# Optimization experiments

Hardware: AMD Instinct MI355X
Metric: run time of the kernel (lower is better)

The kernel has to match this reference:

```python
import jax, jax.numpy as jnp
import numpy as np

D = 256

def setup_inputs() -> dict:
    key = jax.random.key(0)
    ks = jax.random.split(key, 7)
    B, N = 4, 4096
    s = 1.0 / np.sqrt(D)
    return {
        "x": jax.random.normal(ks[0], (B, D, N), dtype=jnp.float32),
        "Wq": jax.random.normal(ks[1], (D, D), dtype=jnp.float32) * s,
        "bq": jax.random.normal(ks[2], (D,), dtype=jnp.float32) * s,
        "Wk": jax.random.normal(ks[3], (D, D), dtype=jnp.float32) * s,
        "bk": jax.random.normal(ks[4], (D,), dtype=jnp.float32) * s,
        "Wv": jax.random.normal(ks[5], (D, D), dtype=jnp.float32) * s,
        "bv": jax.random.normal(ks[6], (D,), dtype=jnp.float32) * s,
    }


def reference(x, Wq, bq, Wk, bk, Wv, bv):
    # x: (B, D, N) -> xt: (B, N, D)
    xt = jnp.swapaxes(x, 1, 2)
    q = xt @ Wq + bq  # (B, N, D)
    k = xt @ Wk + bk
    v = xt @ Wv + bv
    # full N x N attention, NO 1/sqrt(d) scaling (matches original)
    attn = jnp.einsum("bnd,bmd->bnm", q, k)
    attn = jax.nn.softmax(attn, axis=-1)
    out = jnp.einsum("bnm,bmd->bnd", attn, v)  # (B, N, D)
    return jnp.swapaxes(out, 1, 2)  # (B, D, N)
```

## Files before the change

kernel.cpp:

```cpp
#include <hip/hip_runtime.h>
#include <math.h>

#define Dd 256
#define Nn 4096
#define Bb 4
#define BQ 128
#define BK 128
#define SPLIT 2

typedef _Float16 f16;
typedef _Float16 half8 __attribute__((ext_vector_type(8)));
typedef _Float16 half4 __attribute__((ext_vector_type(4)));
typedef float f32x4 __attribute__((ext_vector_type(4)));

#define LOG2E 1.4426950408889634f

template <int CTRL>
__device__ __forceinline__ float dppf(float x) {
    int r = __builtin_amdgcn_update_dpp(0, __builtin_bit_cast(int, x),
                                        CTRL, 0xF, 0xF, false);
    return __builtin_bit_cast(float, r);
}
__device__ __forceinline__ float red16_max(float x) {
    x = fmaxf(x, dppf<0x128>(x));
    x = fmaxf(x, dppf<0x124>(x));
    x = fmaxf(x, dppf<0x122>(x));
    x = fmaxf(x, dppf<0x121>(x));
    return x;
}
__device__ __forceinline__ float red16_sum(float x) {
    x += dppf<0x128>(x); x += dppf<0x124>(x);
    x += dppf<0x122>(x); x += dppf<0x121>(x);
    return x;
}

__global__ __launch_bounds__(256) void wtrans(
    const float* __restrict__ Wq, const float* __restrict__ Wk,
    const float* __restrict__ Wv, f16* __restrict__ Wt)
{
    __shared__ float ld[64][65];
    const int which = blockIdx.y;
    const float* W = which == 0 ? Wq : (which == 1 ? Wk : Wv);
    const int tr = (blockIdx.x >> 2) * 64;
    const int tc = (blockIdx.x & 3) * 64;
    const int t = threadIdx.x;
    #pragma unroll
    for (int i = 0; i < 16; ++i) {
        int u = t + i * 256, r = u >> 6, c = u & 63;
        ld[r][c] = W[(size_t)(tr + r) * Dd + tc + c];
    }
    __syncthreads();
    f16* Wo = Wt + (size_t)which * Dd * Dd;
    #pragma unroll
    for (int i = 0; i < 16; ++i) {
        int u = t + i * 256, cp = u >> 6, rp = u & 63;
        Wo[(size_t)(tc + cp) * Dd + tr + rp] = (f16)ld[rp][cp];
    }
}

__global__ __launch_bounds__(512, 1) void qkv_fused(
    const float* __restrict__ x, const f16* __restrict__ Wt,
    const float* __restrict__ bq, const float* __restrict__ bk,
    const float* __restrict__ bv,
    f16* __restrict__ Qh, f16* __restrict__ Kh, f16* __restrict__ Vth)
{
    __shared__ __align__(16) f16 Ws[256][264];
    __shared__ float bs3[3][256];
    f16 (*xT)[264] = (f16 (*)[264])&Ws[0][0];

    const int t = threadIdx.x;
    const int wave = t >> 6, lane = t & 63, quad = lane >> 4, l15 = lane & 15;
    const int g = wave & 3;
    const int h = wave >> 2;
    const int n0 = blockIdx.x * 64;
    const int b = blockIdx.y;

    if (t < 256) { bs3[0][t] = bq[t]; bs3[1][t] = bk[t]; bs3[2][t] = bv[t]; }

    const float* xb = x + (size_t)b * Dd * Nn;
    #pragma unroll
    for (int i = 0; i < 8; ++i) {
        int u = t + i * 512, d = u >> 4, nq = (u & 15) * 4;
        float4 v4 = *(const float4*)&xb[(size_t)d * Nn + n0 + nq];
        xT[nq + 0][d] = (f16)v4.x; xT[nq + 1][d] = (f16)v4.y;
        xT[nq + 2][d] = (f16)v4.z; xT[nq + 3][d] = (f16)v4.w;
    }
    __syncthreads();

    half8 a[8];
    #pragma unroll
    for (int c = 0; c < 8; ++c)
        a[c] = *(const half8*)&xT[16 * g + l15][c * 32 + quad * 8];

    const int nrow = n0 + 16 * g + quad * 4;

    for (int which = 0; which < 3; ++which) {
        __syncthreads();

        const f16* Wb = Wt + (size_t)which * Dd * Dd;
        #pragma unroll
        for (int i = 0; i < 16; ++i) {
            int u = t + i * 512;
            int r = u >> 5, c = u & 31;
            *(half8*)&Ws[r][c * 8] = *(const half8*)(Wb + (size_t)r * Dd + c * 8);
        }
        __syncthreads();

        f32x4 acc[8];
        #pragma unroll
        for (int dt = 0; dt < 8; ++dt) acc[dt] = (f32x4){0.f, 0.f, 0.f, 0.f};
        #pragma unroll
        for (int c = 0; c < 8; ++c) {
            #pragma unroll
            for (int dt = 0; dt < 8; ++dt) {
                half8 bfr = *(const half8*)&Ws[h * 128 + dt * 16 + l15][c * 32 + quad * 8];
                acc[dt] = __builtin_amdgcn_mfma_f32_16x16x32_f16(a[c], bfr, acc[dt], 0, 0, 0);
            }
        }

        if (which < 2) {
            f16* O = (which == 0 ? Qh : Kh) + ((size_t)b * Nn + nrow) * Dd;
            #pragma unroll
            for (int dt = 0; dt < 8; ++dt) {
                int col = h * 128 + dt * 16 + l15;
                float bvv = bs3[which][col];
                #pragma unroll
                for (int r = 0; r < 4; ++r)
                    O[(size_t)r * Dd + col] = (f16)(acc[dt][r] + bvv);
            }
        } else {
            f16* O = Vth + (size_t)b * Dd * Nn;
            #pragma unroll
            for (int dt = 0; dt < 8; ++dt) {
                int col = h * 128 + dt * 16 + l15;
                float bvv = bs3[2][col];
                half4 o;
                #pragma unroll
                for (int r = 0; r < 4; ++r) o[r] = (f16)(acc[dt][r] + bvv);
                *(half4*)&O[(size_t)col * Nn + nrow] = o;
            }
        }
    }
}

__global__ __launch_bounds__(512, 2) void attn_mfma(
    const f16* __restrict__ Qh, const f16* __restrict__ Kh,
    const f16* __restrict__ Vth, f16* __restrict__ Opart,
    float* __restrict__ mpart, float* __restrict__ lpart)
{
    __shared__ f16 Ks[BK][264];
    __shared__ f16 Ps[8][16][136];
    __shared__ float alpha_s[8][16];
    __shared__ float l_sh[8][16];

    const int t    = threadIdx.x;
    const int wave = t >> 6, lane = t & 63;
    const int quad = lane >> 4, l15 = lane & 15;
    const int b    = blockIdx.y;
    const int s    = blockIdx.z;
    const int q0   = blockIdx.x * BQ;
    const int qw   = q0 + wave * 16;
    const int kv0  = s * (Nn / SPLIT);

    half8 qf[8];
    const f16* Qrow = Qh + ((size_t)b * Nn + qw + l15) * Dd + quad * 8;
    #pragma unroll
    for (int c = 0; c < 8; ++c) {
        qf[c] = *(const half8*)(Qrow + c * 32);
        qf[c] = qf[c] * (f16)LOG2E;
    }

    f32x4 acc[16];
    #pragma unroll
    for (int n = 0; n < 16; ++n) acc[n] = (f32x4){0.f, 0.f, 0.f, 0.f};
    f32x4 m4 = {-1e30f, -1e30f, -1e30f, -1e30f};
    f32x4 l4 = {0.f, 0.f, 0.f, 0.f};

    const f16* Kb   = Kh + (size_t)b * Nn * Dd;
    const f16* Vrow = Vth + (size_t)b * Dd * Nn
                    + (size_t)(wave * 32 + l15) * Nn + quad * 8;

    for (int k0 = kv0; k0 < kv0 + Nn / SPLIT; k0 += BK) {
        half8 vbf[2][4];
        #pragma unroll
        for (int dt = 0; dt < 2; ++dt) {
            #pragma unroll
            for (int cbb = 0; cbb < 4; ++cbb)
                vbf[dt][cbb] = *(const half8*)(Vrow + (size_t)dt * 16 * Nn + k0 + cbb * 32);
        }

        __syncthreads();

        #pragma unroll
        for (int i = 0; i < 8; ++i) {
            int u = t + i * 512;
            int r = u >> 5, c = u & 31;
            *(half8*)&Ks[r][c * 8] =
                *(const half8*)(Kb + (size_t)(k0 + r) * Dd + c * 8);
        }
        __syncthreads();

        f32x4 S[8];
        #pragma unroll
        for (int cb = 0; cb < 8; ++cb) S[cb] = (f32x4){0.f, 0.f, 0.f, 0.f};
        #pragma unroll
        for (int c = 0; c < 8; ++c) {
            #pragma unroll
            for (int cb = 0; cb < 8; ++cb) {
                half8 kb = *(const half8*)&Ks[cb * 16 + l15][c * 32 + quad * 8];
                S[cb] = __builtin_amdgcn_mfma_f32_16x16x32_f16(qf[c], kb, S[cb], 0, 0, 0);
            }
        }

        f32x4 tmax = S[0];
        #pragma unroll
        for (int cb = 1; cb < 8; ++cb) {
            tmax.x = fmaxf(tmax.x, S[cb].x); tmax.y = fmaxf(tmax.y, S[cb].y);
            tmax.z = fmaxf(tmax.z, S[cb].z); tmax.w = fmaxf(tmax.w, S[cb].w);
        }
        tmax.x = red16_max(tmax.x); tmax.y = red16_max(tmax.y);
        tmax.z = red16_max(tmax.z); tmax.w = red16_max(tmax.w);
        f32x4 newm;
        newm.x = fmaxf(m4.x, tmax.x); newm.y = fmaxf(m4.y, tmax.y);
        newm.z = fmaxf(m4.z, tmax.z); newm.w = fmaxf(m4.w, tmax.w);
        f32x4 al;
        al.x = __builtin_amdgcn_exp2f(m4.x - newm.x);
        al.y = __builtin_amdgcn_exp2f(m4.y - newm.y);
        al.z = __builtin_amdgcn_exp2f(m4.z - newm.z);
        al.w = __builtin_amdgcn_exp2f(m4.w - newm.w);
        f32x4 P[8];
        #pragma unroll
        for (int cb = 0; cb < 8; ++cb) {
            P[cb].x = __builtin_amdgcn_exp2f(S[cb].x - newm.x);
            P[cb].y = __builtin_amdgcn_exp2f(S[cb].y - newm.y);
            P[cb].z = __builtin_amdgcn_exp2f(S[cb].z - newm.z);
            P[cb].w = __builtin_amdgcn_exp2f(S[cb].w - newm.w);
        }
        f32x4 rsum = P[0];
        #pragma unroll
        for (int cb = 1; cb < 8; ++cb) rsum += P[cb];
        rsum.x = red16_sum(rsum.x); rsum.y = red16_sum(rsum.y);
        rsum.z = red16_sum(rsum.z); rsum.w = red16_sum(rsum.w);
        l4 = l4 * al + rsum;
        m4 = newm;

        const int pr = quad * 4;
        #pragma unroll
        for (int cb = 0; cb < 8; ++cb) {
            Ps[wave][pr + 0][cb * 16 + l15] = (f16)P[cb].x;
            Ps[wave][pr + 1][cb * 16 + l15] = (f16)P[cb].y;
            Ps[wave][pr + 2][cb * 16 + l15] = (f16)P[cb].z;
            Ps[wave][pr + 3][cb * 16 + l15] = (f16)P[cb].w;
        }
        if (l15 == 0) {
            float4 a4 = {al.x, al.y, al.z, al.w};
            *(float4*)&alpha_s[wave][pr] = a4;
        }
        __syncthreads();

        float4 alq[8];
        int need = 0;
        #pragma unroll
        for (int qb = 0; qb < 8; ++qb) {
            alq[qb] = *(const float4*)&alpha_s[qb][pr];
            need |= (alq[qb].x != 1.f) | (alq[qb].y != 1.f) |
                    (alq[qb].z != 1.f) | (alq[qb].w != 1.f);
        }
        if (__any(need)) {
            #pragma unroll
            for (int qb = 0; qb < 8; ++qb) {
                f32x4 a = {alq[qb].x, alq[qb].y, alq[qb].z, alq[qb].w};
                acc[qb * 2 + 0] *= a;
                acc[qb * 2 + 1] *= a;
            }
        }

        #pragma unroll
        for (int qb = 0; qb < 8; ++qb) {
            #pragma unroll
            for (int cbb = 0; cbb < 4; ++cbb) {
                half8 ap = *(const half8*)&Ps[qb][l15][cbb * 32 + quad * 8];
                acc[qb * 2 + 0] = __builtin_amdgcn_mfma_f32_16x16x32_f16(
                    ap, vbf[0][cbb], acc[qb * 2 + 0], 0, 0, 0);
                acc[qb * 2 + 1] = __builtin_amdgcn_mfma_f32_16x16x32_f16(
                    ap, vbf[1][cbb], acc[qb * 2 + 1], 0, 0, 0);
            }
        }
    }

    __syncthreads();
    if (l15 == 0) {
        const int pr = quad * 4;
        float4 lv = {l4.x, l4.y, l4.z, l4.w};
        *(float4*)&l_sh[wave][pr] = lv;
        float mv[4] = {m4.x, m4.y, m4.z, m4.w};
        float lvv[4] = {l4.x, l4.y, l4.z, l4.w};
        #pragma unroll
        for (int r = 0; r < 4; ++r) {
            int n = qw + pr + r;
            mpart[(size_t)(s * Bb + b) * Nn + n] = mv[r];
            lpart[(size_t)(s * Bb + b) * Nn + n] = lvv[r];
        }
    }
    __syncthreads();

    f16* Ob = Opart + (size_t)(s * Bb + b) * Dd * Nn;
    #pragma unroll
    for (int qb = 0; qb < 8; ++qb) {
        float4 lq = *(const float4*)&l_sh[qb][quad * 4];
        f32x4 inv = {1.f / lq.x, 1.f / lq.y, 1.f / lq.z, 1.f / lq.w};
        #pragma unroll
        for (int dt = 0; dt < 2; ++dt) {
            int d = wave * 32 + dt * 16 + l15;
            f32x4 o = acc[qb * 2 + dt] * inv;
            half4 oh;
            oh[0] = (f16)o.x; oh[1] = (f16)o.y; oh[2] = (f16)o.z; oh[3] = (f16)o.w;
            *(half4*)&Ob[(size_t)d * Nn + q0 + qb * 16 + quad * 4] = oh;
        }
    }
}

__global__ __launch_bounds__(256) void combine(
    const f16* __restrict__ Opart, const float* __restrict__ mpart,
    const float* __restrict__ lpart, float* __restrict__ out)
{
    const int t = threadIdx.x;
    const int n0 = (blockIdx.x * 256 + t) * 8;
    const int d = blockIdx.y, b = blockIdx.z;

    float m[SPLIT][8], l[SPLIT][8];
    #pragma unroll
    for (int s = 0; s < SPLIT; ++s) {
        size_t base = (size_t)(s * Bb + b) * Nn + n0;
        float4 a0 = *(const float4*)&mpart[base];
        float4 a1 = *(const float4*)&mpart[base + 4];
        float4 c0 = *(const float4*)&lpart[base];
        float4 c1 = *(const float4*)&lpart[base + 4];
        m[s][0]=a0.x; m[s][1]=a0.y; m[s][2]=a0.z; m[s][3]=a0.w;
        m[s][4]=a1.x; m[s][5]=a1.y; m[s][6]=a1.z; m[s][7]=a1.w;
        l[s][0]=c0.x; l[s][1]=c0.y; l[s][2]=c0.z; l[s][3]=c0.w;
        l[s][4]=c1.x; l[s][5]=c1.y; l[s][6]=c1.z; l[s][7]=c1.w;
    }
    float w[SPLIT][8];
    #pragma unroll
    for (int jx = 0; jx < 8; ++jx) {
        float M = m[0][jx];
        #pragma unroll
        for (int s = 1; s < SPLIT; ++s) M = fmaxf(M, m[s][jx]);
        float L = 0.f;
        #pragma unroll
        for (int s = 0; s < SPLIT; ++s) {
            float ws = l[s][jx] * __builtin_amdgcn_exp2f(m[s][jx] - M);
            w[s][jx] = ws; L += ws;
        }
        float invL = 1.f / L;
        #pragma unroll
        for (int s = 0; s < SPLIT; ++s) w[s][jx] *= invL;
    }

    float o[8];
    #pragma unroll
    for (int jx = 0; jx < 8; ++jx) o[jx] = 0.f;
    #pragma unroll
    for (int s = 0; s < SPLIT; ++s) {
        half8 h = *(const half8*)&Opart[((size_t)(s * Bb + b) * Dd + d) * Nn + n0];
        #pragma unroll
        for (int jx = 0; jx < 8; ++jx) o[jx] += w[s][jx] * (float)h[jx];
    }
    float* op = out + ((size_t)b * Dd + d) * Nn + n0;
    f32x4 o0 = {o[0], o[1], o[2], o[3]};
    f32x4 o1 = {o[4], o[5], o[6], o[7]};
    *(f32x4*)op = o0;
    *(f32x4*)(op + 4) = o1;
}

extern "C" void kernel_launch(void* const* d_in, const int* in_sizes, int n_in,
                              void* d_out, int out_size, void* d_ws, size_t ws_size,
                              hipStream_t stream) {
    const float* x  = (const float*)d_in[0];
    const float* Wq = (const float*)d_in[1];
    const float* bq = (const float*)d_in[2];
    const float* Wk = (const float*)d_in[3];
    const float* bk = (const float*)d_in[4];
    const float* Wv = (const float*)d_in[5];
    const float* bv = (const float*)d_in[6];
    float* out = (float*)d_out;

    f16* Qh    = (f16*)d_ws;
    f16* Kh    = Qh + (size_t)Bb * Nn * Dd;
    f16* Vth   = Kh + (size_t)Bb * Nn * Dd;
    f16* Wt    = Vth + (size_t)Bb * Nn * Dd;
    f16* Opart = Wt + (size_t)3 * Dd * Dd;
    float* mpart = (float*)(Opart + (size_t)SPLIT * Bb * Dd * Nn);
    float* lpart = mpart + (size_t)SPLIT * Bb * Nn;

    wtrans<<<dim3(16, 3), 256, 0, stream>>>(Wq, Wk, Wv, Wt);
    qkv_fused<<<dim3(Nn / 64, Bb), 512, 0, stream>>>(
        x, Wt, bq, bk, bv, Qh, Kh, Vth);
    attn_mfma<<<dim3(Nn / BQ, Bb, SPLIT), 512, 0, stream>>>(
        Qh, Kh, Vth, Opart, mpart, lpart);
    combine<<<dim3(Nn / 2048, Dd, Bb), 256, 0, stream>>>(
        Opart, mpart, lpart, out);
}
```

Before: 219.8 us.

## Raise KV split to four when workspace allows and alias P buffer onto K tile

Makes the KV split count a runtime choice: four when the workspace can hold the extra partial outputs, otherwise two. The attention grid therefore grows from 256 to 512 blocks and combine is templated on the split count. The P tile now reuses the K tile's shared memory, which needs an extra barrier before P is written. This shrinks LDS per block so more blocks may fit per CU, at the cost of more partial-output traffic and a heavier combine pass.

```diff
diff --git a/kernel.cpp b/kernel.cpp
--- a/kernel.cpp
+++ b/kernel.cpp
@@ -6,7 +6,6 @@
 #define Bb 4
 #define BQ 128
 #define BK 128
-#define SPLIT 2
 
 typedef _Float16 f16;
 typedef _Float16 half8 __attribute__((ext_vector_type(8)));
@@ -146,12 +145,12 @@
 __global__ __launch_bounds__(512, 2) void attn_mfma(
     const f16* __restrict__ Qh, const f16* __restrict__ Kh,
     const f16* __restrict__ Vth, f16* __restrict__ Opart,
-    float* __restrict__ mpart, float* __restrict__ lpart)
+    float* __restrict__ mpart, float* __restrict__ lpart, int kvlen)
 {
-    __shared__ f16 Ks[BK][264];
-    __shared__ f16 Ps[8][16][136];
+    __shared__ __align__(16) f16 Ks[BK][264];
     __shared__ float alpha_s[8][16];
     __shared__ float l_sh[8][16];
+    f16 (*Ps)[16][136] = (f16 (*)[16][136])&Ks[0][0];
 
     const int t    = threadIdx.x;
     const int wave = t >> 6, lane = t & 63;
@@ -160,7 +159,7 @@
     const int s    = blockIdx.z;
     const int q0   = blockIdx.x * BQ;
     const int qw   = q0 + wave * 16;
-    const int kv0  = s * (Nn / SPLIT);
+    const int kv0  = s * kvlen;
 
     half8 qf[8];
     const f16* Qrow = Qh + ((size_t)b * Nn + qw + l15) * Dd + quad * 8;
@@ -180,7 +179,7 @@
     const f16* Vrow = Vth + (size_t)b * Dd * Nn
                     + (size_t)(wave * 32 + l15) * Nn + quad * 8;
 
-    for (int k0 = kv0; k0 < kv0 + Nn / SPLIT; k0 += BK) {
+    for (int k0 = kv0; k0 < kv0 + kvlen; k0 += BK) {
         half8 vbf[2][4];
         #pragma unroll
         for (int dt = 0; dt < 2; ++dt) {
@@ -244,6 +243,8 @@
         l4 = l4 * al + rsum;
         m4 = newm;
 
+        __syncthreads();
+
         const int pr = quad * 4;
         #pragma unroll
         for (int cb = 0; cb < 8; ++cb) {
@@ -320,6 +321,7 @@
     }
 }
 
+template <int S>
 __global__ __launch_bounds__(256) void combine(
     const f16* __restrict__ Opart, const float* __restrict__ mpart,
     const float* __restrict__ lpart, float* __restrict__ out)
@@ -328,9 +330,9 @@
     const int n0 = (blockIdx.x * 256 + t) * 8;
     const int d = blockIdx.y, b = blockIdx.z;
 
-    float m[SPLIT][8], l[SPLIT][8];
-    #pragma unroll
-    for (int s = 0; s < SPLIT; ++s) {
+    float m[S][8], l[S][8];
+    #pragma unroll
+    for (int s = 0; s < S; ++s) {
         size_t base = (size_t)(s * Bb + b) * Nn + n0;
         float4 a0 = *(const float4*)&mpart[base];
         float4 a1 = *(const float4*)&mpart[base + 4];
@@ -341,28 +343,28 @@
         l[s][0]=c0.x; l[s][1]=c0.y; l[s][2]=c0.z; l[s][3]=c0.w;
         l[s][4]=c1.x; l[s][5]=c1.y; l[s][6]=c1.z; l[s][7]=c1.w;
     }
-    float w[SPLIT][8];
+    float w[S][8];
     #pragma unroll
     for (int jx = 0; jx < 8; ++jx) {
         float M = m[0][jx];
         #pragma unroll
-        for (int s = 1; s < SPLIT; ++s) M = fmaxf(M, m[s][jx]);
+        for (int s = 1; s < S; ++s) M = fmaxf(M, m[s][jx]);
         float L = 0.f;
         #pragma unroll
-        for (int s = 0; s < SPLIT; ++s) {
+        for (int s = 0; s < S; ++s) {
             float ws = l[s][jx] * __builtin_amdgcn_exp2f(m[s][jx] - M);
             w[s][jx] = ws; L += ws;
         }
         float invL = 1.f / L;
         #pragma unroll
-        for (int s = 0; s < SPLIT; ++s) w[s][jx] *= invL;
+        for (int s = 0; s < S; ++s) w[s][jx] *= invL;
     }
 
     float o[8];
     #pragma unroll
     for (int jx = 0; jx < 8; ++jx) o[jx] = 0.f;
     #pragma unroll
-    for (int s = 0; s < SPLIT; ++s) {
+    for (int s = 0; s < S; ++s) {
         half8 h = *(const half8*)&Opart[((size_t)(s * Bb + b) * Dd + d) * Nn + n0];
         #pragma unroll
         for (int jx = 0; jx < 8; ++jx) o[jx] += w[s][jx] * (float)h[jx];
@@ -386,19 +388,29 @@
     const float* bv = (const float*)d_in[6];
     float* out = (float*)d_out;
 
+    const size_t head = (size_t)3 * Bb * Nn * Dd * sizeof(f16)
+                      + (size_t)3 * Dd * Dd * sizeof(f16);
+    const size_t per_split = (size_t)Bb * Dd * Nn * sizeof(f16)
+                           + 2 * (size_t)Bb * Nn * sizeof(float);
+    int split = (head + 4 * per_split <= ws_size) ? 4 : 2;
+
     f16* Qh    = (f16*)d_ws;
     f16* Kh    = Qh + (size_t)Bb * Nn * Dd;
     f16* Vth   = Kh + (size_t)Bb * Nn * Dd;
     f16* Wt    = Vth + (size_t)Bb * Nn * Dd;
     f16* Opart = Wt + (size_t)3 * Dd * Dd;
-    float* mpart = (float*)(Opart + (size_t)SPLIT * Bb * Dd * Nn);
-    float* lpart = mpart + (size_t)SPLIT * Bb * Nn;
+    float* mpart = (float*)(Opart + (size_t)split * Bb * Dd * Nn);
+    float* lpart = mpart + (size_t)split * Bb * Nn;
 
     wtrans<<<dim3(16, 3), 256, 0, stream>>>(Wq, Wk, Wv, Wt);
     qkv_fused<<<dim3(Nn / 64, Bb), 512, 0, stream>>>(
         x, Wt, bq, bk, bv, Qh, Kh, Vth);
-    attn_mfma<<<dim3(Nn / BQ, Bb, SPLIT), 512, 0, stream>>>(
-        Qh, Kh, Vth, Opart, mpart, lpart);
-    combine<<<dim3(Nn / 2048, Dd, Bb), 256, 0, stream>>>(
-        Opart, mpart, lpart, out);
-}
+    attn_mfma<<<dim3(Nn / BQ, Bb, split), 512, 0, stream>>>(
+        Qh, Kh, Vth, Opart, mpart, lpart, Nn / split);
+    if (split == 4)
+        combine<4><<<dim3(Nn / 2048, Dd, Bb), 256, 0, stream>>>(
+            Opart, mpart, lpart, out);
+    else
+        combine<2><<<dim3(Nn / 2048, Dd, Bb), 256, 0, stream>>>(
+            Opart, mpart, lpart, out);
+}
```

Measured after the change: 237.1 us. +7.9%, slower.

## Double-buffer K tile via register prefetch and alias P buffer onto consumed K

Applied to the files above, without the earlier changes.

Loads the next K tile into registers at the start of each iteration and writes it to the alternate shared-memory buffer after the PV matmul, so global latency overlaps compute. The P staging area now reuses the current K buffer once the QK^T product is finished, which keeps shared-memory usage roughly flat despite double buffering. The change adds 8 half8 registers per thread, which could push register pressure past the launch bound of 2 blocks per CU, and it rearranges barriers around the aliased buffer.

```diff
diff --git a/kernel.cpp b/kernel.cpp
--- a/kernel.cpp
+++ b/kernel.cpp
@@ -148,8 +148,7 @@
     const f16* __restrict__ Vth, f16* __restrict__ Opart,
     float* __restrict__ mpart, float* __restrict__ lpart)
 {
-    __shared__ f16 Ks[BK][264];
-    __shared__ f16 Ps[8][16][136];
+    __shared__ __align__(16) f16 Ks[2][BK][264];
     __shared__ float alpha_s[8][16];
     __shared__ float l_sh[8][16];
 
@@ -160,7 +159,8 @@
     const int s    = blockIdx.z;
     const int q0   = blockIdx.x * BQ;
     const int qw   = q0 + wave * 16;
-    const int kv0  = s * (Nn / SPLIT);
+    const int kvlen = Nn / SPLIT;
+    const int kv0  = s * kvlen;
 
     half8 qf[8];
     const f16* Qrow = Qh + ((size_t)b * Nn + qw + l15) * Dd + quad * 8;
@@ -180,7 +180,29 @@
     const f16* Vrow = Vth + (size_t)b * Dd * Nn
                     + (size_t)(wave * 32 + l15) * Nn + quad * 8;
 
-    for (int k0 = kv0; k0 < kv0 + Nn / SPLIT; k0 += BK) {
+    #pragma unroll
+    for (int i = 0; i < 8; ++i) {
+        int u = t + i * 512;
+        int r = u >> 5, c = u & 31;
+        *(half8*)&Ks[0][r][c * 8] =
+            *(const half8*)(Kb + (size_t)(kv0 + r) * Dd + c * 8);
+    }
+    __syncthreads();
+
+    int buf = 0;
+    for (int k0 = kv0; k0 < kv0 + kvlen; k0 += BK) {
+        const int kn = k0 + BK;
+        const bool havenext = kn < kv0 + kvlen;
+        half8 kreg[8];
+        if (havenext) {
+            #pragma unroll
+            for (int i = 0; i < 8; ++i) {
+                int u = t + i * 512;
+                int r = u >> 5, c = u & 31;
+                kreg[i] = *(const half8*)(Kb + (size_t)(kn + r) * Dd + c * 8);
+            }
+        }
+
         half8 vbf[2][4];
         #pragma unroll
         for (int dt = 0; dt < 2; ++dt) {
@@ -189,17 +211,6 @@
                 vbf[dt][cbb] = *(const half8*)(Vrow + (size_t)dt * 16 * Nn + k0 + cbb * 32);
         }
 
-        __syncthreads();
-
-        #pragma unroll
-        for (int i = 0; i < 8; ++i) {
-            int u = t + i * 512;
-            int r = u >> 5, c = u & 31;
-            *(half8*)&Ks[r][c * 8] =
-                *(const half8*)(Kb + (size_t)(k0 + r) * Dd + c * 8);
-        }
-        __syncthreads();
-
         f32x4 S[8];
         #pragma unroll
         for (int cb = 0; cb < 8; ++cb) S[cb] = (f32x4){0.f, 0.f, 0.f, 0.f};
@@ -207,7 +218,7 @@
         for (int c = 0; c < 8; ++c) {
             #pragma unroll
             for (int cb = 0; cb < 8; ++cb) {
-                half8 kb = *(const half8*)&Ks[cb * 16 + l15][c * 32 + quad * 8];
+                half8 kb = *(const half8*)&Ks[buf][cb * 16 + l15][c * 32 + quad * 8];
                 S[cb] = __builtin_amdgcn_mfma_f32_16x16x32_f16(qf[c], kb, S[cb], 0, 0, 0);
             }
         }
@@ -228,29 +239,31 @@
         al.y = __builtin_amdgcn_exp2f(m4.y - newm.y);
         al.z = __builtin_amdgcn_exp2f(m4.z - newm.z);
         al.w = __builtin_amdgcn_exp2f(m4.w - newm.w);
-        f32x4 P[8];
         #pragma unroll
         for (int cb = 0; cb < 8; ++cb) {
-            P[cb].x = __builtin_amdgcn_exp2f(S[cb].x - newm.x);
-            P[cb].y = __builtin_amdgcn_exp2f(S[cb].y - newm.y);
-            P[cb].z = __builtin_amdgcn_exp2f(S[cb].z - newm.z);
-            P[cb].w = __builtin_amdgcn_exp2f(S[cb].w - newm.w);
-        }
-        f32x4 rsum = P[0];
-        #pragma unroll
-        for (int cb = 1; cb < 8; ++cb) rsum += P[cb];
+            S[cb].x = __builtin_amdgcn_exp2f(S[cb].x - newm.x);
+            S[cb].y = __builtin_amdgcn_exp2f(S[cb].y - newm.y);
+            S[cb].z = __builtin_amdgcn_exp2f(S[cb].z - newm.z);
+            S[cb].w = __builtin_amdgcn_exp2f(S[cb].w - newm.w);
+        }
+        f32x4 rsum = S[0];
+        #pragma unroll
+        for (int cb = 1; cb < 8; ++cb) rsum += S[cb];
         rsum.x = red16_sum(rsum.x); rsum.y = red16_sum(rsum.y);
         rsum.z = red16_sum(rsum.z); rsum.w = red16_sum(rsum.w);
         l4 = l4 * al + rsum;
         m4 = newm;
 
+        __syncthreads();
+
+        f16 (*Ps)[16][136] = (f16 (*)[16][136])&Ks[buf][0][0];
         const int pr = quad * 4;
         #pragma unroll
         for (int cb = 0; cb < 8; ++cb) {
-            Ps[wave][pr + 0][cb * 16 + l15] = (f16)P[cb].x;
-            Ps[wave][pr + 1][cb * 16 + l15] = (f16)P[cb].y;
-            Ps[wave][pr + 2][cb * 16 + l15] = (f16)P[cb].z;
-            Ps[wave][pr + 3][cb * 16 + l15] = (f16)P[cb].w;
+            Ps[wave][pr + 0][cb * 16 + l15] = (f16)S[cb].x;
+            Ps[wave][pr + 1][cb * 16 + l15] = (f16)S[cb].y;
+            Ps[wave][pr + 2][cb * 16 + l15] = (f16)S[cb].z;
+            Ps[wave][pr + 3][cb * 16 + l15] = (f16)S[cb].w;
         }
         if (l15 == 0) {
             float4 a4 = {al.x, al.y, al.z, al.w};
@@ -286,9 +299,19 @@
                     ap, vbf[1][cbb], acc[qb * 2 + 1], 0, 0, 0);
             }
         }
-    }
-
-    __syncthreads();
+
+        if (havenext) {
+            #pragma unroll
+            for (int i = 0; i < 8; ++i) {
+                int u = t + i * 512;
+                int r = u >> 5, c = u & 31;
+                *(half8*)&Ks[buf ^ 1][r][c * 8] = kreg[i];
+            }
+            buf ^= 1;
+        }
+        __syncthreads();
+    }
+
     if (l15 == 0) {
         const int pr = quad * 4;
         float4 lv = {l4.x, l4.y, l4.z, l4.w};
```

Result: faster. 210.5 us (-4.2%).
